# Optimization experiments

Measured on AMD Instinct MI355X. Metric: run time of the kernel, lower is better.

## Reference

```python
import jax, jax.numpy as jnp
import numpy as np

EMBED_DIM = 512
NUM_HEADS = 8
HEAD_DIM = EMBED_DIM // NUM_HEADS
ATTN_STD = 1.0          # attn_param for attn_type='normal'
# attn_position='center' => no displacement of query indices


def setup_inputs() -> dict:
    key = jax.random.key(0)
    k1, k2, k3 = jax.random.split(key, 3)
    B, S = 4, 4096
    inputs = jax.random.normal(k1, (B, S, EMBED_DIM), dtype=jnp.float32)
    # xavier-uniform-like scale for [E, E] weights
    bound = np.float32(np.sqrt(6.0 / (EMBED_DIM + EMBED_DIM)))
    input_weights = jax.random.uniform(k2, (EMBED_DIM, EMBED_DIM), jnp.float32, -bound, bound)
    output_weight = jax.random.uniform(k3, (EMBED_DIM, EMBED_DIM), jnp.float32, -bound, bound)
    return {"inputs": inputs, "input_weights": input_weights, "output_weight": output_weight}


def _gaussian_weights(s_q, s_v, dtype):
    # logits[i, j] = 1/(std*sqrt(2*pi)) * exp(-0.5*((j-i)/std)^2)
    iq = jnp.arange(s_q, dtype=dtype)[:, None]
    iv = jnp.arange(s_v, dtype=dtype)[None, :]
    diff = iv - iq
    coef = (1.0 / (ATTN_STD * np.sqrt(2.0 * np.pi))).astype(np.float32)
    return coef * jnp.exp(-0.5 * (diff / ATTN_STD) ** 2)


def reference(inputs, input_weights, output_weight):
    B, S, E = inputs.shape
    H, D = NUM_HEADS, HEAD_DIM
    # project(): F.linear(inputs, input_weights) then split heads -> [B*H, S, D]
    v = jnp.einsum('bse,fe->bsf', inputs, input_weights)
    v = v.reshape(B, S, H, D).transpose(0, 2, 1, 3).reshape(B * H, S, D)
    # hard-coded Gaussian positional attention weights [S, S] (data independent)
    w = _gaussian_weights(S, S, inputs.dtype).astype(v.dtype)
    attended = jnp.einsum('qk,nkd->nqd', w, v)  # bmm with broadcast weights
    attended = attended.reshape(B, H, S, D).transpose(0, 2, 1, 3).reshape(B, S, E)
    # output_projection: Linear(E, E, bias=False)
    return jnp.einsum('bse,fe->bsf', attended, output_weight)
```

## Files before the change

### kernel.cpp

```cpp
#include <hip/hip_runtime.h>
#include <hip/hip_bf16.h>


typedef unsigned short u16;
typedef unsigned int u32;
typedef unsigned long long u64;
typedef __attribute__((ext_vector_type(8))) short bf16x8;
typedef __attribute__((ext_vector_type(8))) unsigned short u16x8;
typedef __attribute__((ext_vector_type(4))) unsigned short u16x4;
typedef __attribute__((ext_vector_type(4))) float f32x4;
typedef __attribute__((ext_vector_type(2))) u32 u32x2;

typedef __attribute__((address_space(1))) const void* as1_cvp;
typedef __attribute__((address_space(3))) void* as3_vp;

#define EDIM 512
#define NROW 16384
#define ROWS_OUT 120
#define MBLK 137
#define NWG (MBLK * 4)
#define NKT 16
#define LA1 5120
#define LBB 10240
#define YSTR 136

__device__ __forceinline__ float b2f(u16 x) {
  union { u32 u; float f; } c; c.u = ((u32)x) << 16; return c.f;
}
__device__ __forceinline__ u16 f2b(float x) {
  union { float f; u32 u; } c; c.f = x;
  return (u16)((c.u + 0x7fffu + ((c.u >> 16) & 1u)) >> 16);
}
__device__ __forceinline__ u32 cvtpk(float lo, float hi) {
  u32 r;
  asm("v_cvt_pk_bf16_f32 %0, %1, %2" : "=v"(r) : "v"(lo), "v"(hi));
  return r;
}
__device__ __forceinline__ void async_cp16(const void* g, void* l) {
  __builtin_amdgcn_global_load_lds((as1_cvp)(u64)g, (as3_vp)(u32)(u64)l, 16, 0, 0);
}

__global__ __launch_bounds__(256) void gemm_m(const float* __restrict__ Wout,
                                              const float* __restrict__ Win,
                                              u16* __restrict__ Mm) {
  __shared__ u16 la[64 * 136];
  __shared__ u16 lbt[64 * 136];
  int t = threadIdx.x;
  int w = t >> 6, l = t & 63, lr = l & 15, lk = l >> 4;
  int f0 = (int)(blockIdx.x >> 3) * 64, e0 = (int)(blockIdx.x & 7) * 64;
  int arow = t >> 2, acol = (t & 3) * 32;
  int brow = t >> 1, bcol = (t & 1) * 32;
  const float* pA = Wout + (u64)(f0 + arow) * EDIM + acol;
  const float* pB = Win + (u64)brow * EDIM + e0 + bcol;
  f32x4 a8[8], b8[8];
#pragma unroll
  for (int i = 0; i < 8; ++i) {
    a8[i] = *(const f32x4*)(pA + i * 4);
    b8[i] = *(const f32x4*)(pB + i * 4);
  }
  f32x4 acc[4] = {};
  for (int kt = 0; kt < 4; ++kt) {
#pragma unroll
    for (int i = 0; i < 4; ++i) {
      u16x8 o;
#pragma unroll
      for (int q = 0; q < 4; ++q) { o[q] = f2b(a8[2 * i][q]); o[4 + q] = f2b(a8[2 * i + 1][q]); }
      *(u16x8*)(la + arow * 136 + acol + i * 8) = o;
    }
#pragma unroll
    for (int i = 0; i < 8; ++i)
#pragma unroll
      for (int q = 0; q < 4; ++q)
        lbt[(bcol + i * 4 + q) * 136 + brow] = f2b(b8[i][q]);
    asm volatile("s_waitcnt lgkmcnt(0)" ::: "memory");
    __builtin_amdgcn_sched_barrier(0);
    __builtin_amdgcn_s_barrier();
    if (kt < 3) {
      pA += 128; pB += (u64)128 * EDIM;
#pragma unroll
      for (int i = 0; i < 8; ++i) {
        a8[i] = *(const f32x4*)(pA + i * 4);
        b8[i] = *(const f32x4*)(pB + i * 4);
      }
    }
#pragma unroll
    for (int kk = 0; kk < 128; kk += 32) {
      bf16x8 a = *(const bf16x8*)(la + (w * 16 + lr) * 136 + kk + lk * 8);
#pragma unroll
      for (int ni = 0; ni < 4; ++ni) {
        bf16x8 bb = *(const bf16x8*)(lbt + (ni * 16 + lr) * 136 + kk + lk * 8);
        acc[ni] = __builtin_amdgcn_mfma_f32_16x16x32_bf16(a, bb, acc[ni], 0, 0, 0);
      }
    }
    asm volatile("s_waitcnt lgkmcnt(0)" ::: "memory");
    __builtin_amdgcn_sched_barrier(0);
    __builtin_amdgcn_s_barrier();
  }
#pragma unroll
  for (int ni = 0; ni < 4; ++ni)
#pragma unroll
    for (int r = 0; r < 4; ++r)
      Mm[(u64)(f0 + w * 16 + lk * 4 + r) * EDIM + e0 + ni * 16 + lr] = f2b(acc[ni][r]);
}

template <bool EDGE>
__device__ __forceinline__ void conv_store(const u16* __restrict__ Y, int t,
                                           int m0c, int n0, float* __restrict__ out) {
  const float G[5] = {0.39894228040143270f, 0.24197072451914337f,
                      0.053990966513188063f, 0.0044318484119380075f,
                      1.3383022576488537e-4f};
  int qc = t & 31, grp = t >> 5;
  int rl0 = 4 + grp * 15;
  const u16* Yb = Y + qc * 4;
  f32x4 wnd[9];
#pragma unroll
  for (int i = 0; i < 9; ++i) {
    u16x4 yv = *(const u16x4*)(Yb + (rl0 - 4 + i) * YSTR);
#pragma unroll
    for (int q = 0; q < 4; ++q) wnd[i][q] = b2f(yv[q]);
  }
#pragma unroll
  for (int j = 0; j < 15; ++j) {
    int rg = m0c + rl0 + j;
    f32x4 a = {};
#pragma unroll
    for (int k = 0; k < 9; ++k) {
      float g = G[k < 4 ? 4 - k : k - 4];
      if (EDGE) {
        int rt = rg + k - 4;
        g = ((rt >> 12) == (rg >> 12)) ? g : 0.0f;
      }
#pragma unroll
      for (int q = 0; q < 4; ++q) a[q] += g * wnd[(j + k) % 9][q];
    }
    if (!EDGE || rg < NROW)
      *(f32x4*)(out + (u64)rg * EDIM + n0 + qc * 4) = a;
    if (j < 14) {
      u16x4 yv = *(const u16x4*)(Yb + (rl0 + j + 5) * YSTR);
#pragma unroll
      for (int q = 0; q < 4; ++q) wnd[j % 9][q] = b2f(yv[q]);
    }
  }
}

#define KSTEP(KT, RL, RC, ARD_, AWR_, BRD_, BWR_, VM)                          \
  {                                                                            \
    async_cp16(bsrc0 + ((KT) + 1) * 32, lds + (BWR_) + t * 8);                 \
    async_cp16(bsrc1 + ((KT) + 1) * 32, lds + (BWR_) + 2048 + t * 8);          \
    __builtin_amdgcn_sched_barrier(0);                                         \
    if ((KT) + 2 < NKT) {                                                      \
      _Pragma("unroll") for (int j = 0; j < 4; ++j)                            \
          RL[j] = *(const f32x4*)(in + rowoff[j] + ((KT) + 2) * 32);           \
    }                                                                          \
    __builtin_amdgcn_sched_barrier(0);                                         \
    bf16x8 af[4], bv[4];                                                       \
    _Pragma("unroll") for (int mi = 0; mi < 4; ++mi)                           \
        af[mi] = *(const bf16x8*)(lds + (ARD_) + ard[mi]);                     \
    _Pragma("unroll") for (int ni = 0; ni < 4; ++ni)                           \
        bv[ni] = *(const bf16x8*)(lds + (BRD_) + brd[ni]);                     \
    _Pragma("unroll") for (int mi = 0; mi < 4; ++mi)                           \
      _Pragma("unroll") for (int ni = 0; ni < 4; ++ni)                         \
          acc[mi][ni] = __builtin_amdgcn_mfma_f32_16x16x32_bf16(               \
              af[mi], bv[ni], acc[mi][ni], 0, 0, 0);                           \
    _Pragma("unroll") for (int j = 0; j < 4; ++j) {                            \
      u32x2 p;                                                                 \
      p[0] = cvtpk(RC[j][0], RC[j][1]);                                        \
      p[1] = cvtpk(RC[j][2], RC[j][3]);                                        \
      *(u32x2*)(lds + (AWR_) + awi[j]) = p;                                    \
    }                                                                          \
    asm volatile("s_waitcnt vmcnt(" #VM ") lgkmcnt(0)" ::: "memory");          \
    __builtin_amdgcn_sched_barrier(0);                                         \
    __builtin_amdgcn_s_barrier();                                              \
  }

__global__ __launch_bounds__(256, 3) void fused_gc(const float* __restrict__ in,
                                                   const u16* __restrict__ Mm,
                                                   float* __restrict__ out) {
  __shared__ u16 lds[18432];
  int t = threadIdx.x;
  int l = t & 63, lr = l & 15, lk = l >> 4;
  int wv = t >> 6, wr = wv >> 1, wc = wv & 1;

  int b = (int)blockIdx.x;
  int q = NWG >> 3, r = NWG & 7;
  int xcd = b & 7, off = b >> 3;
  int wg = (xcd < r ? xcd * (q + 1) : r * (q + 1) + (xcd - r) * q) + off;
  int ib = wg >> 2;
  int n0 = (wg & 3) << 7;
  int m0c = ib * ROWS_OUT - 4;

  u32 rowoff[4];
#pragma unroll
  for (int j = 0; j < 4; ++j) {
    int rg = m0c + j * 32 + (t >> 3);
    rg = rg < 0 ? 0 : (rg > NROW - 1 ? NROW - 1 : rg);
    rowoff[j] = (u32)rg * EDIM + (t & 7) * 4;
  }
  int brow0 = t >> 2, slot = t & 3;
  int brow1 = brow0 + 64;
  const u16* bsrc0 = Mm + (u64)(n0 + brow0) * EDIM + ((slot ^ ((brow0 ^ (brow0 >> 2)) & 3)) * 8);
  const u16* bsrc1 = Mm + (u64)(n0 + brow1) * EDIM + ((slot ^ ((brow1 ^ (brow1 >> 2)) & 3)) * 8);

  int awi[4];
#pragma unroll
  for (int j = 0; j < 4; ++j) awi[j] = (j * 32 + (t >> 3)) * 40 + (t & 7) * 4;
  int ard[4], brd[4];
#pragma unroll
  for (int mi = 0; mi < 4; ++mi) ard[mi] = (wr * 64 + mi * 16 + lr) * 40 + lk * 8;
#pragma unroll
  for (int ni = 0; ni < 4; ++ni) {
    int row = wc * 64 + ni * 16 + lr;
    brd[ni] = (row * 32 + lk * 8) ^ (((row ^ (row >> 2)) & 3) << 3);
  }

  f32x4 acc[4][4] = {};
  f32x4 rP[4], rQ[4];

#pragma unroll
  for (int j = 0; j < 4; ++j) rP[j] = *(const f32x4*)(in + rowoff[j]);
  __builtin_amdgcn_sched_barrier(0);
#pragma unroll
  for (int j = 0; j < 4; ++j) {
    u32x2 p;
    p[0] = cvtpk(rP[j][0], rP[j][1]);
    p[1] = cvtpk(rP[j][2], rP[j][3]);
    *(u32x2*)(lds + awi[j]) = p;
  }
  __builtin_amdgcn_sched_barrier(0);
  async_cp16(bsrc0, lds + LBB + t * 8);
  async_cp16(bsrc1, lds + LBB + 2048 + t * 8);
  __builtin_amdgcn_sched_barrier(0);
#pragma unroll
  for (int j = 0; j < 4; ++j) rQ[j] = *(const f32x4*)(in + rowoff[j] + 32);
  __builtin_amdgcn_sched_barrier(0);
  asm volatile("s_waitcnt vmcnt(4) lgkmcnt(0)" ::: "memory");
  __builtin_amdgcn_sched_barrier(0);
  __builtin_amdgcn_s_barrier();

  for (int kt = 0; kt < 14; kt += 2) {
    KSTEP(kt,     rP, rQ, 0,   LA1, LBB,        LBB + 4096, 4)
    KSTEP(kt + 1, rQ, rP, LA1, 0,   LBB + 4096, LBB,        4)
  }
  KSTEP(14, rP, rQ, 0, LA1, LBB, LBB + 4096, 0)
  {
    bf16x8 af[4], bv[4];
#pragma unroll
    for (int mi = 0; mi < 4; ++mi) af[mi] = *(const bf16x8*)(lds + LA1 + ard[mi]);
#pragma unroll
    for (int ni = 0; ni < 4; ++ni) bv[ni] = *(const bf16x8*)(lds + LBB + 4096 + brd[ni]);
#pragma unroll
    for (int mi = 0; mi < 4; ++mi)
#pragma unroll
      for (int ni = 0; ni < 4; ++ni)
        acc[mi][ni] = __builtin_amdgcn_mfma_f32_16x16x32_bf16(af[mi], bv[ni],
                                                              acc[mi][ni], 0, 0, 0);
  }
  __syncthreads();

  u16* Y = lds;
#pragma unroll
  for (int mi = 0; mi < 4; ++mi)
#pragma unroll
    for (int ni = 0; ni < 4; ++ni)
#pragma unroll
      for (int rr = 0; rr < 4; ++rr)
        Y[(wr * 64 + mi * 16 + lk * 4 + rr) * YSTR + wc * 64 + ni * 16 + lr] =
            f2b(acc[mi][ni][rr]);
  __syncthreads();

  bool edge = ((m0c >> 12) != ((m0c + 127) >> 12));
  if (edge)
    conv_store<true>(Y, t, m0c, n0, out);
  else
    conv_store<false>(Y, t, m0c, n0, out);
}

extern "C" void kernel_launch(void* const* d_in, const int* in_sizes, int n_in,
                              void* d_out, int out_size, void* d_ws, size_t ws_size,
                              hipStream_t stream) {
  const float* in   = (const float*)d_in[0];
  const float* Win  = (const float*)d_in[1];
  const float* Wout = (const float*)d_in[2];
  float* outp = (float*)d_out;

  u16* Mm = (u16*)d_ws;

  hipLaunchKernelGGL(gemm_m,   dim3(64), dim3(256), 0, stream, Wout, Win, Mm);
  hipLaunchKernelGGL(fused_gc, dim3(NWG), dim3(256), 0, stream, in, Mm, outp);
}
```

Baseline: 40.07 us.

## Load A operand fragments directly into registers, bypassing LDS staging

```diff
diff --git a/kernel.cpp b/kernel.cpp
--- a/kernel.cpp
+++ b/kernel.cpp
@@ -19,9 +19,6 @@
 #define ROWS_OUT 120
 #define MBLK 137
 #define NWG (MBLK * 4)
-#define NKT 16
-#define LA1 5120
-#define LBB 10240
 #define YSTR 136
 
 __device__ __forceinline__ float b2f(u16 x) {
@@ -39,6 +36,7 @@
 __device__ __forceinline__ void async_cp16(const void* g, void* l) {
   __builtin_amdgcn_global_load_lds((as1_cvp)(u64)g, (as3_vp)(u32)(u64)l, 16, 0, 0);
 }
+union bfu { u32 w[4]; bf16x8 v; };
 
 __global__ __launch_bounds__(256) void gemm_m(const float* __restrict__ Wout,
                                               const float* __restrict__ Win,
@@ -49,14 +47,16 @@
   int w = t >> 6, l = t & 63, lr = l & 15, lk = l >> 4;
   int f0 = (int)(blockIdx.x >> 3) * 64, e0 = (int)(blockIdx.x & 7) * 64;
   int arow = t >> 2, acol = (t & 3) * 32;
-  int brow = t >> 1, bcol = (t & 1) * 32;
+  int cq = t >> 3, eo = (t & 7) * 8;
   const float* pA = Wout + (u64)(f0 + arow) * EDIM + acol;
-  const float* pB = Win + (u64)brow * EDIM + e0 + bcol;
+  const float* pB = Win + (u64)(4 * cq) * EDIM + e0 + eo;
   f32x4 a8[8], b8[8];
 #pragma unroll
-  for (int i = 0; i < 8; ++i) {
-    a8[i] = *(const f32x4*)(pA + i * 4);
-    b8[i] = *(const f32x4*)(pB + i * 4);
+  for (int i = 0; i < 8; ++i) a8[i] = *(const f32x4*)(pA + i * 4);
+#pragma unroll
+  for (int r = 0; r < 4; ++r) {
+    b8[r * 2 + 0] = *(const f32x4*)(pB + r * EDIM);
+    b8[r * 2 + 1] = *(const f32x4*)(pB + r * EDIM + 4);
   }
   f32x4 acc[4] = {};
   for (int kt = 0; kt < 4; ++kt) {
@@ -68,19 +68,23 @@
       *(u16x8*)(la + arow * 136 + acol + i * 8) = o;
     }
 #pragma unroll
-    for (int i = 0; i < 8; ++i)
-#pragma unroll
-      for (int q = 0; q < 4; ++q)
-        lbt[(bcol + i * 4 + q) * 136 + brow] = f2b(b8[i][q]);
+    for (int j = 0; j < 8; ++j) {
+      u32x2 p;
+      p[0] = cvtpk(b8[0 + (j >> 2)][j & 3], b8[2 + (j >> 2)][j & 3]);
+      p[1] = cvtpk(b8[4 + (j >> 2)][j & 3], b8[6 + (j >> 2)][j & 3]);
+      *(u32x2*)(lbt + (eo + j) * 136 + 4 * cq) = p;
+    }
     asm volatile("s_waitcnt lgkmcnt(0)" ::: "memory");
     __builtin_amdgcn_sched_barrier(0);
     __builtin_amdgcn_s_barrier();
     if (kt < 3) {
       pA += 128; pB += (u64)128 * EDIM;
 #pragma unroll
-      for (int i = 0; i < 8; ++i) {
-        a8[i] = *(const f32x4*)(pA + i * 4);
-        b8[i] = *(const f32x4*)(pB + i * 4);
+      for (int i = 0; i < 8; ++i) a8[i] = *(const f32x4*)(pA + i * 4);
+#pragma unroll
+      for (int r = 0; r < 4; ++r) {
+        b8[r * 2 + 0] = *(const f32x4*)(pB + r * EDIM);
+        b8[r * 2 + 1] = *(const f32x4*)(pB + r * EDIM + 4);
       }
     }
 #pragma unroll
@@ -143,40 +147,44 @@
   }
 }
 
-#define KSTEP(KT, RL, RC, ARD_, AWR_, BRD_, BWR_, VM)                          \
+#define KSTEP(KT, S0, S1, BCUR, BNXT, VM)                                      \
   {                                                                            \
-    async_cp16(bsrc0 + ((KT) + 1) * 32, lds + (BWR_) + t * 8);                 \
-    async_cp16(bsrc1 + ((KT) + 1) * 32, lds + (BWR_) + 2048 + t * 8);          \
-    __builtin_amdgcn_sched_barrier(0);                                         \
-    if ((KT) + 2 < NKT) {                                                      \
-      _Pragma("unroll") for (int j = 0; j < 4; ++j)                            \
-          RL[j] = *(const f32x4*)(in + rowoff[j] + ((KT) + 2) * 32);           \
+    bf16x8 af[4];                                                              \
+    _Pragma("unroll") for (int mi = 0; mi < 4; ++mi) {                         \
+      bfu u_;                                                                  \
+      u_.w[0] = cvtpk(S0[mi][0], S0[mi][1]);                                   \
+      u_.w[1] = cvtpk(S0[mi][2], S0[mi][3]);                                   \
+      u_.w[2] = cvtpk(S1[mi][0], S1[mi][1]);                                   \
+      u_.w[3] = cvtpk(S1[mi][2], S1[mi][3]);                                   \
+      af[mi] = u_.v;                                                           \
     }                                                                          \
     __builtin_amdgcn_sched_barrier(0);                                         \
-    bf16x8 af[4], bv[4];                                                       \
-    _Pragma("unroll") for (int mi = 0; mi < 4; ++mi)                           \
-        af[mi] = *(const bf16x8*)(lds + (ARD_) + ard[mi]);                     \
+    async_cp16(bsrc0 + ((KT) + 1) * 32, lds + (BNXT) + t * 8);                 \
+    async_cp16(bsrc1 + ((KT) + 1) * 32, lds + (BNXT) + 2048 + t * 8);          \
+    __builtin_amdgcn_sched_barrier(0);                                         \
+    if ((KT) + 2 < 16) {                                                       \
+      _Pragma("unroll") for (int mi = 0; mi < 4; ++mi) {                       \
+        S0[mi] = *(const f32x4*)(in + rowA[mi] + ((KT) + 2) * 32);             \
+        S1[mi] = *(const f32x4*)(in + rowA[mi] + ((KT) + 2) * 32 + 4);         \
+      }                                                                        \
+    }                                                                          \
+    __builtin_amdgcn_sched_barrier(0);                                         \
+    bf16x8 bv[4];                                                              \
     _Pragma("unroll") for (int ni = 0; ni < 4; ++ni)                           \
-        bv[ni] = *(const bf16x8*)(lds + (BRD_) + brd[ni]);                     \
+        bv[ni] = *(const bf16x8*)(lds + (BCUR) + brd[ni]);                     \
     _Pragma("unroll") for (int mi = 0; mi < 4; ++mi)                           \
       _Pragma("unroll") for (int ni = 0; ni < 4; ++ni)                         \
           acc[mi][ni] = __builtin_amdgcn_mfma_f32_16x16x32_bf16(               \
               af[mi], bv[ni], acc[mi][ni], 0, 0, 0);                           \
-    _Pragma("unroll") for (int j = 0; j < 4; ++j) {                            \
-      u32x2 p;                                                                 \
-      p[0] = cvtpk(RC[j][0], RC[j][1]);                                        \
-      p[1] = cvtpk(RC[j][2], RC[j][3]);                                        \
-      *(u32x2*)(lds + (AWR_) + awi[j]) = p;                                    \
-    }                                                                          \
-    asm volatile("s_waitcnt vmcnt(" #VM ") lgkmcnt(0)" ::: "memory");          \
+    asm volatile("s_waitcnt vmcnt(" #VM ")" ::: "memory");                     \
     __builtin_amdgcn_sched_barrier(0);                                         \
     __builtin_amdgcn_s_barrier();                                              \
   }
 
-__global__ __launch_bounds__(256, 3) void fused_gc(const float* __restrict__ in,
+__global__ __launch_bounds__(256, 2) void fused_gc(const float* __restrict__ in,
                                                    const u16* __restrict__ Mm,
                                                    float* __restrict__ out) {
-  __shared__ u16 lds[18432];
+  __shared__ u16 lds[17408];
   int t = threadIdx.x;
   int l = t & 63, lr = l & 15, lk = l >> 4;
   int wv = t >> 6, wr = wv >> 1, wc = wv & 1;
@@ -189,24 +197,18 @@
   int n0 = (wg & 3) << 7;
   int m0c = ib * ROWS_OUT - 4;
 
-  u32 rowoff[4];
-#pragma unroll
-  for (int j = 0; j < 4; ++j) {
-    int rg = m0c + j * 32 + (t >> 3);
+  u32 rowA[4];
+#pragma unroll
+  for (int mi = 0; mi < 4; ++mi) {
+    int rg = m0c + wr * 64 + mi * 16 + lr;
     rg = rg < 0 ? 0 : (rg > NROW - 1 ? NROW - 1 : rg);
-    rowoff[j] = (u32)rg * EDIM + (t & 7) * 4;
+    rowA[mi] = (u32)rg * EDIM + lk * 8;
   }
   int brow0 = t >> 2, slot = t & 3;
   int brow1 = brow0 + 64;
   const u16* bsrc0 = Mm + (u64)(n0 + brow0) * EDIM + ((slot ^ ((brow0 ^ (brow0 >> 2)) & 3)) * 8);
   const u16* bsrc1 = Mm + (u64)(n0 + brow1) * EDIM + ((slot ^ ((brow1 ^ (brow1 >> 2)) & 3)) * 8);
-
-  int awi[4];
-#pragma unroll
-  for (int j = 0; j < 4; ++j) awi[j] = (j * 32 + (t >> 3)) * 40 + (t & 7) * 4;
-  int ard[4], brd[4];
-#pragma unroll
-  for (int mi = 0; mi < 4; ++mi) ard[mi] = (wr * 64 + mi * 16 + lr) * 40 + lk * 8;
+  int brd[4];
 #pragma unroll
   for (int ni = 0; ni < 4; ++ni) {
     int row = wc * 64 + ni * 16 + lr;
@@ -214,40 +216,43 @@
   }
 
   f32x4 acc[4][4] = {};
-  f32x4 rP[4], rQ[4];
-
-#pragma unroll
-  for (int j = 0; j < 4; ++j) rP[j] = *(const f32x4*)(in + rowoff[j]);
-  __builtin_amdgcn_sched_barrier(0);
-#pragma unroll
-  for (int j = 0; j < 4; ++j) {
-    u32x2 p;
-    p[0] = cvtpk(rP[j][0], rP[j][1]);
-    p[1] = cvtpk(rP[j][2], rP[j][3]);
-    *(u32x2*)(lds + awi[j]) = p;
-  }
-  __builtin_amdgcn_sched_barrier(0);
-  async_cp16(bsrc0, lds + LBB + t * 8);
-  async_cp16(bsrc1, lds + LBB + 2048 + t * 8);
-  __builtin_amdgcn_sched_barrier(0);
-#pragma unroll
-  for (int j = 0; j < 4; ++j) rQ[j] = *(const f32x4*)(in + rowoff[j] + 32);
-  __builtin_amdgcn_sched_barrier(0);
-  asm volatile("s_waitcnt vmcnt(4) lgkmcnt(0)" ::: "memory");
+  f32x4 aP0[4], aP1[4], aQ0[4], aQ1[4];
+
+#pragma unroll
+  for (int mi = 0; mi < 4; ++mi) {
+    aP0[mi] = *(const f32x4*)(in + rowA[mi]);
+    aP1[mi] = *(const f32x4*)(in + rowA[mi] + 4);
+  }
+#pragma unroll
+  for (int mi = 0; mi < 4; ++mi) {
+    aQ0[mi] = *(const f32x4*)(in + rowA[mi] + 32);
+    aQ1[mi] = *(const f32x4*)(in + rowA[mi] + 36);
+  }
+  async_cp16(bsrc0, lds + t * 8);
+  async_cp16(bsrc1, lds + 2048 + t * 8);
+  asm volatile("s_waitcnt vmcnt(0)" ::: "memory");
   __builtin_amdgcn_sched_barrier(0);
   __builtin_amdgcn_s_barrier();
 
   for (int kt = 0; kt < 14; kt += 2) {
-    KSTEP(kt,     rP, rQ, 0,   LA1, LBB,        LBB + 4096, 4)
-    KSTEP(kt + 1, rQ, rP, LA1, 0,   LBB + 4096, LBB,        4)
-  }
-  KSTEP(14, rP, rQ, 0, LA1, LBB, LBB + 4096, 0)
+    KSTEP(kt,     aP0, aP1, 0,    4096, 8)
+    KSTEP(kt + 1, aQ0, aQ1, 4096, 0,    8)
+  }
+  KSTEP(14, aP0, aP1, 0, 4096, 0)
   {
-    bf16x8 af[4], bv[4];
-#pragma unroll
-    for (int mi = 0; mi < 4; ++mi) af[mi] = *(const bf16x8*)(lds + LA1 + ard[mi]);
-#pragma unroll
-    for (int ni = 0; ni < 4; ++ni) bv[ni] = *(const bf16x8*)(lds + LBB + 4096 + brd[ni]);
+    bf16x8 af[4];
+#pragma unroll
+    for (int mi = 0; mi < 4; ++mi) {
+      bfu u_;
+      u_.w[0] = cvtpk(aQ0[mi][0], aQ0[mi][1]);
+      u_.w[1] = cvtpk(aQ0[mi][2], aQ0[mi][3]);
+      u_.w[2] = cvtpk(aQ1[mi][0], aQ1[mi][1]);
+      u_.w[3] = cvtpk(aQ1[mi][2], aQ1[mi][3]);
+      af[mi] = u_.v;
+    }
+    bf16x8 bv[4];
+#pragma unroll
+    for (int ni = 0; ni < 4; ++ni) bv[ni] = *(const bf16x8*)(lds + 4096 + brd[ni]);
 #pragma unroll
     for (int mi = 0; mi < 4; ++mi)
 #pragma unroll
```

After: 68.86 us. 1.72x slower.
